# Kernel tuning notes

Hardware: AMD Instinct MI355X
Metric: run time of the kernel (lower is better)

The kernel has to match this reference:

```python
import jax, jax.numpy as jnp
import numpy as np
from jax import lax

T, B, C, H, W, NH = 4, 4, 512, 32, 32, 8
HD = C // NH  # head dim 64
EPS = 1e-5
TAU = 2.0

@jax.custom_vjp
def spike(x):
    # Heaviside forward (spikingjelly: x >= 0 -> 1)
    return (x >= 0.0).astype(x.dtype)

def _spike_fwd(x):
    return spike(x), x

def _spike_bwd(x, g):
    # sigmoid surrogate gradient, alpha=4.0 (spikingjelly default)
    s = jax.nn.sigmoid(4.0 * x)
    return (g * 4.0 * s * (1.0 - s),)

spike.defvjp(_spike_fwd, _spike_bwd)

def lif(x, v_th=1.0):
    # MultiStepLIFNode: tau=2, v_reset=0 (hard reset), detach_reset=True.
    # x: [T, ...]; sequential over T via scan.
    def step(v, xt):
        v = v + (xt - v) / TAU
        s = spike(v - v_th)
        v = v * (1.0 - lax.stop_gradient(s))  # detach_reset hard reset
        return v, s
    return lax.scan(step, jnp.zeros_like(x[0]), x)[1]

def bn(x, g, b, m, v):
    # eval-mode BatchNorm1d over channel axis 2 of [T,B,C,N]
    scale = g / jnp.sqrt(v + EPS)
    return (x - m[:, None]) * scale[:, None] + b[:, None]

def setup_inputs() -> dict:
    key = jax.random.key(0)
    ks = jax.random.split(key, 24)
    def w(k):
        return jax.random.normal(k, (C, C), jnp.float32) * (1.0 / np.sqrt(C))
    def bnp(k):
        k1, k2, k3, k4 = jax.random.split(k, 4)
        return (jax.random.normal(k1, (C,), jnp.float32) * 0.1 + 1.0,
                jax.random.normal(k2, (C,), jnp.float32) * 0.1,
                jax.random.normal(k3, (C,), jnp.float32) * 0.1,
                jax.random.uniform(k4, (C,), jnp.float32, 0.5, 1.5))
    q_g, q_b, q_m, q_v = bnp(ks[1])
    k_g, k_b, k_m, k_v = bnp(ks[3])
    v_g, v_b, v_m, v_v = bnp(ks[5])
    p_g, p_b, p_m, p_v = bnp(ks[7])
    return {
        'x': jax.random.normal(ks[0], (T, B, C, H, W), jnp.float32),
        'Wq': w(ks[10]), 'q_g': q_g, 'q_b': q_b, 'q_m': q_m, 'q_v': q_v,
        'Wk': w(ks[11]), 'k_g': k_g, 'k_b': k_b, 'k_m': k_m, 'k_v': k_v,
        'Wv': w(ks[12]), 'v_g': v_g, 'v_b': v_b, 'v_m': v_m, 'v_v': v_v,
        'Wp': w(ks[13]), 'bp': jax.random.normal(ks[14], (C,), jnp.float32) * 0.02,
        'p_g': p_g, 'p_b': p_b, 'p_m': p_m, 'p_v': p_v,
    }

def reference(x, Wq, q_g, q_b, q_m, q_v, Wk, k_g, k_b, k_m, k_v,
              Wv, v_g, v_b, v_m, v_v, Wp, bp, p_g, p_b, p_m, p_v):
    t, b, c, h, w = x.shape
    n = h * w
    xs = lif(x).reshape(t, b, c, n)  # proj_lif -> spikes in {0,1}

    def qkv_branch(Wt, g, bb, m, v):
        y = jnp.einsum('tbcn,dc->tbdn', xs, Wt)  # conv1x1
        y = lif(bn(y, g, bb, m, v))               # bn + lif
        # [T,B,C,N] -> [T,B,heads,N,head_dim]
        return y.reshape(t, b, NH, HD, n).transpose(0, 1, 2, 4, 3)

    q = qkv_branch(Wq, q_g, q_b, q_m, q_v)
    k = qkv_branch(Wk, k_g, k_b, k_m, k_v)
    v = qkv_branch(Wv, v_g, v_b, v_m, v_v)

    attn = jnp.einsum('tbhnd,tbhmd->tbhnm', q, k)           # q @ k^T (binary spikes)
    o = jnp.einsum('tbhnm,tbhmd->tbhnd', attn, v) * 0.125   # attn @ v * 0.125
    o = o.transpose(0, 1, 2, 4, 3).reshape(t, b, c, n)      # [T,B,C,N]
    o = lif(o, v_th=0.5)                                     # attn_lif

    y = jnp.einsum('tbcn,dc->tbdn', o, Wp) + bp[:, None]     # proj conv (bias)
    y = bn(y, p_g, p_b, p_m, p_v)
    return y.reshape(t, b, c, h, w)
```

## Files before the change

kernel.cpp:

```cpp
#include <hip/hip_runtime.h>
#include <hip/hip_bf16.h>
#include <stdint.h>

#define T_  4
#define B_  4
#define C_  512
#define N_  1024
#define NH_ 8
#define HD_ 64
#define NP_ 16384
#define EPS_ 1e-5f

typedef __bf16 bf16_t;
typedef __bf16 bf16x8 __attribute__((ext_vector_type(8)));
typedef float  f32x4  __attribute__((ext_vector_type(4)));
typedef unsigned short u16x4 __attribute__((ext_vector_type(4)));
typedef unsigned char  u8x4  __attribute__((ext_vector_type(4)));
typedef unsigned long long u64;
typedef unsigned int u32;

#define XS_OFF   0ULL
#define AHI_OFF  16777216ULL
#define ALO_OFF  18350080ULL
#define PHI_OFF  19922944ULL
#define PLO_OFF  20447232ULL
#define SC_OFF   20971520ULL
#define SH_OFF   20977664ULL
#define PSC_OFF  20983808ULL
#define PSH_OFF  20985856ULL
#define QS_OFF   20987904ULL
#define KB_OFF   37765120ULL
#define VB_OFF   38813696ULL
#define M2H_OFF  39862272ULL
#define M2L_OFF  40910848ULL

__global__ __launch_bounds__(256) void prep_lif_kernel(
    const float* __restrict__ x, bf16_t* __restrict__ xsT,
    const float* __restrict__ Wq, const float* __restrict__ Wk,
    const float* __restrict__ Wv, const float* __restrict__ Wp,
    const float* __restrict__ qg, const float* __restrict__ qb, const float* __restrict__ qm, const float* __restrict__ qv,
    const float* __restrict__ kg, const float* __restrict__ kb, const float* __restrict__ km, const float* __restrict__ kv,
    const float* __restrict__ vg, const float* __restrict__ vb, const float* __restrict__ vm, const float* __restrict__ vv,
    const float* __restrict__ bp,
    const float* __restrict__ pg, const float* __restrict__ pb, const float* __restrict__ pm, const float* __restrict__ pv,
    bf16_t* __restrict__ Ahi, bf16_t* __restrict__ Alo,
    bf16_t* __restrict__ Phi, bf16_t* __restrict__ Plo,
    float* __restrict__ scale, float* __restrict__ shift,
    float* __restrict__ pscale, float* __restrict__ pshift)
{
    __shared__ bf16_t St[64 * 72];
    const int tid = threadIdx.x;

    if (blockIdx.z == 4) {
        const int i0 = (blockIdx.y * 16 + blockIdx.x) * 256 + tid;
        const int stride = 128 * 256;
        for (int idx = i0; idx < 1536 * 512; idx += stride) {
            int r = idx >> 9;
            int br = r >> 9;
            const float* W = (br == 0) ? Wq : (br == 1) ? Wk : Wv;
            float w = W[((r & 511) << 9) + (idx & 511)];
            bf16_t h = (bf16_t)w;
            Ahi[idx] = h;
            Alo[idx] = (bf16_t)(w - (float)h);
        }
        for (int idx = i0; idx < 512 * 512; idx += stride) {
            float w = Wp[idx];
            bf16_t h = (bf16_t)w;
            Phi[idx] = h;
            Plo[idx] = (bf16_t)(w - (float)h);
        }
        for (int idx = i0; idx < 1536; idx += stride) {
            int br = idx >> 9, d = idx & 511;
            const float* g  = (br == 0) ? qg : (br == 1) ? kg : vg;
            const float* bb = (br == 0) ? qb : (br == 1) ? kb : vb;
            const float* mm = (br == 0) ? qm : (br == 1) ? km : vm;
            const float* vr = (br == 0) ? qv : (br == 1) ? kv : vv;
            float sc = g[d] / sqrtf(vr[d] + EPS_);
            scale[idx] = sc;
            shift[idx] = bb[d] - mm[d] * sc;
        }
        for (int idx = i0; idx < 512; idx += stride) {
            float sc = pg[idx] / sqrtf(pv[idx] + EPS_);
            pscale[idx] = sc;
            pshift[idx] = (bp[idx] - pm[idx]) * sc + pb[idx];
        }
        return;
    }

    const int nl  = tid & 63;
    const int c4  = tid >> 6;
    const int n0 = blockIdx.x * 64;
    const int c0 = blockIdx.y * 64;
    const int b  = blockIdx.z;
    float v[16];
#pragma unroll
    for (int k = 0; k < 16; ++k) v[k] = 0.f;

    for (int t = 0; t < T_; ++t) {
        bf16x8 s0, s1;
#pragma unroll
        for (int k = 0; k < 16; ++k) {
            float xv = x[(size_t)((t * B_ + b) * C_ + (c0 + c4 * 16 + k)) * N_ + n0 + nl];
            float vn = v[k] + (xv - v[k]) * 0.5f;
            bool s = (vn >= 1.0f);
            v[k] = s ? 0.0f : vn;
            bf16_t sp = s ? (bf16_t)1.0f : (bf16_t)0.0f;
            if (k < 8) s0[k] = sp; else s1[k - 8] = sp;
        }
        __syncthreads();
        *(bf16x8*)&St[nl * 72 + c4 * 16]     = s0;
        *(bf16x8*)&St[nl * 72 + c4 * 16 + 8] = s1;
        __syncthreads();
#pragma unroll
        for (int it = 0; it < 2; ++it) {
            int id = it * 256 + tid;
            int row = id >> 3, sg = id & 7;
            *(bf16x8*)&xsT[((size_t)((t * B_ + b) << 10) + n0 + row) * C_ + c0 + sg * 8] =
                *(const bf16x8*)&St[row * 72 + sg * 8];
        }
    }
}

__global__ __launch_bounds__(256) void gemm_qkv_lif(
    const bf16_t* __restrict__ Ahi, const bf16_t* __restrict__ Alo,
    const bf16_t* __restrict__ xsT,
    const float* __restrict__ scale, const float* __restrict__ shift,
    bf16_t* __restrict__ qsT, u32* __restrict__ kbits, u32* __restrict__ vbits)
{
    __shared__ __align__(16) unsigned char smem[49152];

    const int tid  = threadIdx.x;
    const int lane = tid & 63;
    const int wv   = tid >> 6;
    const int wr   = wv >> 1, wc = wv & 1;
    const int m0   = blockIdx.y * 128;
    const int branch = m0 >> 9;
    const int site0 = blockIdx.x * 32;
    const int b    = site0 >> 10;
    const int n0   = site0 & 1023;

    const int frow = lane & 15;
    const int g4   = lane >> 4;

    f32x4 acc[4][4];
#pragma unroll
    for (int t = 0; t < 4; ++t)
#pragma unroll
        for (int mi = 0; mi < 4; ++mi) acc[t][mi] = f32x4{0.f, 0.f, 0.f, 0.f};

    for (int kk = 0; kk < 512; kk += 64) {
        __syncthreads();
#pragma unroll
        for (int p = 0; p < 4; ++p) {
            int s = p * 256 + tid;
            int row = s >> 3, j = s & 7;
            int kc = (j ^ (row & 7)) << 3;
            size_t goff = (size_t)(m0 + row) * 512 + kk + kc;
            unsigned ldsb = (unsigned)(p * 256 + wv * 64) * 16;
            __builtin_amdgcn_global_load_lds((const __attribute__((address_space(1))) void*)(Ahi + goff),
                                             (__attribute__((address_space(3))) void*)(smem + ldsb), 16, 0, 0);
            __builtin_amdgcn_global_load_lds((const __attribute__((address_space(1))) void*)(Alo + goff),
                                             (__attribute__((address_space(3))) void*)(smem + 16384 + ldsb), 16, 0, 0);
        }
#pragma unroll
        for (int p = 0; p < 4; ++p) {
            int s = p * 256 + tid;
            int t = s >> 8, row = (s >> 3) & 31, j = s & 7;
            int kc = (j ^ (row & 7)) << 3;
            size_t goff = ((size_t)((t * B_ + b) << 10) + n0 + row) * 512 + kk + kc;
            unsigned ldsb = 32768u + (unsigned)(p * 256 + wv * 64) * 16;
            __builtin_amdgcn_global_load_lds((const __attribute__((address_space(1))) void*)(xsT + goff),
                                             (__attribute__((address_space(3))) void*)(smem + ldsb), 16, 0, 0);
        }
        __syncthreads();

#pragma unroll
        for (int ks = 0; ks < 2; ++ks) {
            bf16x8 ah[4], al[4];
#pragma unroll
            for (int mi = 0; mi < 4; ++mi) {
                int row = wr * 64 + mi * 16 + frow;
                int jj = (ks * 4 + g4) ^ (row & 7);
                ah[mi] = *(const bf16x8*)(smem + row * 128 + jj * 16);
                al[mi] = *(const bf16x8*)(smem + 16384 + row * 128 + jj * 16);
            }
#pragma unroll
            for (int t = 0; t < 4; ++t) {
                int rowb = wc * 16 + frow;
                int jj = (ks * 4 + g4) ^ (rowb & 7);
                bf16x8 bb = *(const bf16x8*)(smem + 32768 + t * 4096 + rowb * 128 + jj * 16);
#pragma unroll
                for (int mi = 0; mi < 4; ++mi) {
                    acc[t][mi] = __builtin_amdgcn_mfma_f32_16x16x32_bf16(ah[mi], bb, acc[t][mi], 0, 0, 0);
                    acc[t][mi] = __builtin_amdgcn_mfma_f32_16x16x32_bf16(al[mi], bb, acc[t][mi], 0, 0, 0);
                }
            }
        }
    }

    if (branch == 0) {
        bf16_t* Tt = (bf16_t*)smem;
        u16x4 qpk[4][4];
#pragma unroll
        for (int mi = 0; mi < 4; ++mi)
#pragma unroll
            for (int r = 0; r < 4; ++r) {
                int gr = m0 + wr * 64 + mi * 16 + g4 * 4 + r;
                float sc = scale[gr], sh = shift[gr];
                float vv = 0.f;
#pragma unroll
                for (int t = 0; t < 4; ++t) {
                    float y = acc[t][mi][r] * sc + sh;
                    float vn = vv + (y - vv) * 0.5f;
                    bool s = (vn >= 1.0f);
                    vv = s ? 0.f : vn;
                    qpk[t][mi][r] = s ? 0x3F80 : 0;
                }
            }
#pragma unroll
        for (int t = 0; t < 4; ++t) {
            const int tb = t * B_ + b;
            __syncthreads();
#pragma unroll
            for (int mi = 0; mi < 4; ++mi) {
                int nl = wc * 16 + frow;
                int cl = wr * 64 + mi * 16 + g4 * 4;
                *(u16x4*)&Tt[nl * 136 + cl] = qpk[t][mi];
            }
            __syncthreads();
#pragma unroll
            for (int it = 0; it < 2; ++it) {
                int id = it * 256 + tid;
                int row = id >> 4, sg = id & 15;
                *(bf16x8*)&qsT[((size_t)(tb << 10) + n0 + row) * 512 + m0 + sg * 8] =
                    *(const bf16x8*)&Tt[row * 136 + sg * 8];
            }
        }
    } else {
        unsigned char* Sb = (unsigned char*)smem;
        u32* bdst = (branch == 1) ? kbits : vbits;
        u8x4 kpk[4][4];
#pragma unroll
        for (int mi = 0; mi < 4; ++mi)
#pragma unroll
            for (int r = 0; r < 4; ++r) {
                int gr = m0 + wr * 64 + mi * 16 + g4 * 4 + r;
                float sc = scale[gr], sh = shift[gr];
                float vv = 0.f;
#pragma unroll
                for (int t = 0; t < 4; ++t) {
                    float y = acc[t][mi][r] * sc + sh;
                    float vn = vv + (y - vv) * 0.5f;
                    bool s = (vn >= 1.0f);
                    vv = s ? 0.f : vn;
                    kpk[t][mi][r] = s ? 1 : 0;
                }
            }
#pragma unroll
        for (int t = 0; t < 4; ++t) {
            const int tb = t * B_ + b;
            __syncthreads();
#pragma unroll
            for (int mi = 0; mi < 4; ++mi) {
                int nl = wc * 16 + frow;
                int cl = wr * 64 + mi * 16 + g4 * 4;
                *(u8x4*)&Sb[nl * 132 + cl] = kpk[t][mi];
            }
            __syncthreads();
#pragma unroll
            for (int i = 0; i < 16; ++i) {
                int item = wv * 16 + i;
                int c = item * 2 + (lane >> 5);
                unsigned char vb_ = Sb[(lane & 31) * 132 + c];
                u64 mask = __ballot(vb_ != 0);
                if (lane == 0) {
                    int r0 = (m0 & 511) + item * 2;
                    int r1 = r0 + 1;
                    bdst[((size_t)(tb * NH_ + (r0 >> 6)) * 64 + (r0 & 63)) * 32 + (n0 >> 5)] = (u32)mask;
                    bdst[((size_t)(tb * NH_ + (r1 >> 6)) * 64 + (r1 & 63)) * 32 + (n0 >> 5)] = (u32)(mask >> 32);
                }
            }
        }
    }
}

__global__ __launch_bounds__(256) void gemm_proj(
    const bf16_t* __restrict__ Phi, const bf16_t* __restrict__ Plo,
    const bf16_t* __restrict__ Bm,
    const float* __restrict__ scale, const float* __restrict__ shift,
    float* __restrict__ out)
{
    __shared__ __align__(16) unsigned char smem[49152];

    const int tid  = threadIdx.x;
    const int lane = tid & 63;
    const int wv   = tid >> 6;
    const int wr   = wv >> 1, wc = wv & 1;
    const int m0   = blockIdx.y * 128;
    const int n0   = blockIdx.x * 128;

    const int frow = lane & 15;
    const int g4   = lane >> 4;

    f32x4 acc[4][4];
#pragma unroll
    for (int i = 0; i < 4; ++i)
#pragma unroll
        for (int j = 0; j < 4; ++j) acc[i][j] = f32x4{0.f, 0.f, 0.f, 0.f};

    for (int kk = 0; kk < 512; kk += 64) {
        __syncthreads();
#pragma unroll
        for (int p = 0; p < 4; ++p) {
            int s = p * 256 + tid;
            int row = s >> 3, j = s & 7;
            int kc = (j ^ (row & 7)) << 3;
            size_t goff = (size_t)(m0 + row) * 512 + kk + kc;
            unsigned ldsb = (unsigned)(p * 256 + wv * 64) * 16;
            __builtin_amdgcn_global_load_lds((const __attribute__((address_space(1))) void*)(Phi + goff),
                                             (__attribute__((address_space(3))) void*)(smem + ldsb), 16, 0, 0);
            __builtin_amdgcn_global_load_lds((const __attribute__((address_space(1))) void*)(Plo + goff),
                                             (__attribute__((address_space(3))) void*)(smem + 16384 + ldsb), 16, 0, 0);
        }
#pragma unroll
        for (int p = 0; p < 4; ++p) {
            int s = p * 256 + tid;
            int row = s >> 3, j = s & 7;
            int kc = (j ^ (row & 7)) << 3;
            size_t goff = (size_t)(n0 + row) * 512 + kk + kc;
            unsigned ldsb = 32768u + (unsigned)(p * 256 + wv * 64) * 16;
            __builtin_amdgcn_global_load_lds((const __attribute__((address_space(1))) void*)(Bm + goff),
                                             (__attribute__((address_space(3))) void*)(smem + ldsb), 16, 0, 0);
        }
        __syncthreads();

#pragma unroll
        for (int ks = 0; ks < 2; ++ks) {
            bf16x8 ah[4], al[4];
#pragma unroll
            for (int mi = 0; mi < 4; ++mi) {
                int row = wr * 64 + mi * 16 + frow;
                int jj = (ks * 4 + g4) ^ (row & 7);
                ah[mi] = *(const bf16x8*)(smem + row * 128 + jj * 16);
                al[mi] = *(const bf16x8*)(smem + 16384 + row * 128 + jj * 16);
            }
#pragma unroll
            for (int ni = 0; ni < 4; ++ni) {
                int site = wc * 64 + ni * 16 + frow;
                int jj = (ks * 4 + g4) ^ (site & 7);
                bf16x8 bb = *(const bf16x8*)(smem + 32768 + site * 128 + jj * 16);
#pragma unroll
                for (int mi = 0; mi < 4; ++mi) {
                    acc[mi][ni] = __builtin_amdgcn_mfma_f32_16x16x32_bf16(ah[mi], bb, acc[mi][ni], 0, 0, 0);
                    acc[mi][ni] = __builtin_amdgcn_mfma_f32_16x16x32_bf16(al[mi], bb, acc[mi][ni], 0, 0, 0);
                }
            }
        }
    }

#pragma unroll
    for (int mi = 0; mi < 4; ++mi)
#pragma unroll
        for (int ni = 0; ni < 4; ++ni)
#pragma unroll
            for (int r = 0; r < 4; ++r) {
                int gr = m0 + wr * 64 + mi * 16 + g4 * 4 + r;
                int gc = n0 + wc * 64 + ni * 16 + frow;
                float vout = acc[mi][ni][r] * scale[gr] + shift[gr];
                int tb = gc >> 10, nn = gc & 1023;
                out[((size_t)(tb * C_ + gr)) * N_ + nn] = vout;
            }
}

__global__ __launch_bounds__(256) void m2t_kernel(const u64* __restrict__ kbit,
                                                  const u64* __restrict__ vbit,
                                                  bf16_t* __restrict__ m2h,
                                                  bf16_t* __restrict__ m2l)
{
    __shared__ u64 Kb[64][17];
    __shared__ u64 Vb[64][17];
    __shared__ float M2f[64][64];
    const int tid = threadIdx.x;
    const int h  = blockIdx.x;
    const int tb = blockIdx.y;

    const u64* kbase = kbit + (size_t)(tb * NH_ + h) * 1024;
    const u64* vbase = vbit + (size_t)(tb * NH_ + h) * 1024;
    for (int i = tid; i < 1024; i += 256) {
        Kb[i >> 4][i & 15] = kbase[i];
        Vb[i >> 4][i & 15] = vbase[i];
    }
    __syncthreads();

    const int d1 = tid >> 2, l2 = tid & 3;
    int cnt[16];
#pragma unroll
    for (int jj = 0; jj < 16; ++jj) cnt[jj] = 0;
    for (int w = 0; w < 16; ++w) {
        u64 kw = Kb[d1][w];
#pragma unroll
        for (int jj = 0; jj < 16; ++jj)
            cnt[jj] += __popcll(kw & Vb[l2 + 4 * jj][w]);
    }
#pragma unroll
    for (int jj = 0; jj < 16; ++jj)
        M2f[d1][l2 + 4 * jj] = (float)cnt[jj] * 0.125f;
    __syncthreads();

    const int d2 = tid >> 2, d1b = (tid & 3) * 16;
    bf16x8 h0, h1, l0, l1;
#pragma unroll
    for (int j = 0; j < 16; ++j) {
        float m = M2f[d1b + j][d2];
        bf16_t hi = (bf16_t)m;
        bf16_t lo = (bf16_t)(m - (float)hi);
        if (j < 8) { h0[j] = hi; l0[j] = lo; } else { h1[j - 8] = hi; l1[j - 8] = lo; }
    }
    size_t base = (size_t)(tb * NH_ + h) * 4096 + tid * 16;
    *(bf16x8*)&m2h[base]     = h0;
    *(bf16x8*)&m2h[base + 8] = h1;
    *(bf16x8*)&m2l[base]     = l0;
    *(bf16x8*)&m2l[base + 8] = l1;
}

__global__ __launch_bounds__(256) void o_kernel(const bf16_t* __restrict__ qsT,
                                                const bf16_t* __restrict__ m2h,
                                                const bf16_t* __restrict__ m2l,
                                                bf16_t* __restrict__ osT)
{
    __shared__ bf16_t Ah[64][72];
    __shared__ bf16_t Al[64][72];
    __shared__ bf16_t Bq[64][72];
    __shared__ bf16_t Ot[64][72];

    const int tid  = threadIdx.x;
    const int lane = tid & 63;
    const int wv   = tid >> 6;
    const int nt = blockIdx.x, h = blockIdx.y, b = blockIdx.z;
    const int n0 = nt * 64;
    const int frow = lane & 15;
    const int g    = lane >> 4;

    float vst[4][4];
#pragma unroll
    for (int mi = 0; mi < 4; ++mi)
#pragma unroll
        for (int r = 0; r < 4; ++r) vst[mi][r] = 0.f;

    for (int t = 0; t < T_; ++t) {
        const int tb = t * B_ + b;
        __syncthreads();
        {
            int row = tid >> 2, col = (tid & 3) * 16;
            size_t gbase = (size_t)(tb * NH_ + h) * 4096 + row * 64 + col;
            *(bf16x8*)&Ah[row][col]     = *(const bf16x8*)&m2h[gbase];
            *(bf16x8*)&Ah[row][col + 8] = *(const bf16x8*)&m2h[gbase + 8];
            *(bf16x8*)&Al[row][col]     = *(const bf16x8*)&m2l[gbase];
            *(bf16x8*)&Al[row][col + 8] = *(const bf16x8*)&m2l[gbase + 8];
        }
#pragma unroll
        for (int it = 0; it < 2; ++it) {
            int id = it * 256 + tid;
            int row = id >> 3, cg = (id & 7) * 8;
            *(bf16x8*)&Bq[row][cg] =
                *(const bf16x8*)&qsT[(size_t)((tb << 10) + n0 + row) * C_ + h * 64 + cg];
        }
        __syncthreads();

        bf16x8 afh[4][2], afl[4][2], bfq[2];
#pragma unroll
        for (int mi = 0; mi < 4; ++mi)
#pragma unroll
            for (int ks = 0; ks < 2; ++ks) {
                afh[mi][ks] = *(const bf16x8*)&Ah[mi * 16 + frow][ks * 32 + g * 8];
                afl[mi][ks] = *(const bf16x8*)&Al[mi * 16 + frow][ks * 32 + g * 8];
            }
#pragma unroll
        for (int ks = 0; ks < 2; ++ks)
            bfq[ks] = *(const bf16x8*)&Bq[wv * 16 + frow][ks * 32 + g * 8];

        f32x4 acc[4];
#pragma unroll
        for (int mi = 0; mi < 4; ++mi) acc[mi] = f32x4{0.f, 0.f, 0.f, 0.f};

#pragma unroll
        for (int ks = 0; ks < 2; ++ks)
#pragma unroll
            for (int mi = 0; mi < 4; ++mi) {
                acc[mi] = __builtin_amdgcn_mfma_f32_16x16x32_bf16(afh[mi][ks], bfq[ks], acc[mi], 0, 0, 0);
                acc[mi] = __builtin_amdgcn_mfma_f32_16x16x32_bf16(afl[mi][ks], bfq[ks], acc[mi], 0, 0, 0);
            }

#pragma unroll
        for (int mi = 0; mi < 4; ++mi) {
            u16x4 pk;
#pragma unroll
            for (int r = 0; r < 4; ++r) {
                float o = acc[mi][r];
                float vn = vst[mi][r] + (o - vst[mi][r]) * 0.5f;
                bool s = (vn >= 0.5f);
                vst[mi][r] = s ? 0.f : vn;
                pk[r] = s ? 0x3F80 : 0;
            }
            *(u16x4*)&Ot[wv * 16 + frow][mi * 16 + g * 4] = pk;
        }
        __syncthreads();

#pragma unroll
        for (int it = 0; it < 2; ++it) {
            int id = it * 256 + tid;
            int row = id >> 3, sg = (id & 7) * 8;
            *(bf16x8*)&osT[(size_t)((tb << 10) + n0 + row) * C_ + h * 64 + sg] =
                *(const bf16x8*)&Ot[row][sg];
        }
    }
}

extern "C" void kernel_launch(void* const* d_in, const int* in_sizes, int n_in,
                              void* d_out, int out_size, void* d_ws, size_t ws_size,
                              hipStream_t stream)
{
    const float* x   = (const float*)d_in[0];
    const float* Wq  = (const float*)d_in[1];
    const float* qg  = (const float*)d_in[2];
    const float* qb  = (const float*)d_in[3];
    const float* qm  = (const float*)d_in[4];
    const float* qv  = (const float*)d_in[5];
    const float* Wk  = (const float*)d_in[6];
    const float* kg  = (const float*)d_in[7];
    const float* kb  = (const float*)d_in[8];
    const float* km  = (const float*)d_in[9];
    const float* kv  = (const float*)d_in[10];
    const float* Wv  = (const float*)d_in[11];
    const float* vg  = (const float*)d_in[12];
    const float* vb  = (const float*)d_in[13];
    const float* vm  = (const float*)d_in[14];
    const float* vv  = (const float*)d_in[15];
    const float* Wp  = (const float*)d_in[16];
    const float* bp  = (const float*)d_in[17];
    const float* pg  = (const float*)d_in[18];
    const float* pb  = (const float*)d_in[19];
    const float* pm  = (const float*)d_in[20];
    const float* pv  = (const float*)d_in[21];

    char* ws = (char*)d_ws;
    bf16_t* xsT    = (bf16_t*)(ws + XS_OFF);
    bf16_t* Ahi    = (bf16_t*)(ws + AHI_OFF);
    bf16_t* Alo    = (bf16_t*)(ws + ALO_OFF);
    bf16_t* Phi    = (bf16_t*)(ws + PHI_OFF);
    bf16_t* Plo    = (bf16_t*)(ws + PLO_OFF);
    float*  scv    = (float*)(ws + SC_OFF);
    float*  shv    = (float*)(ws + SH_OFF);
    float*  psc    = (float*)(ws + PSC_OFF);
    float*  psh    = (float*)(ws + PSH_OFF);
    bf16_t* qsT    = (bf16_t*)(ws + QS_OFF);
    u32*    kbits32= (u32*)(ws + KB_OFF);
    u32*    vbits32= (u32*)(ws + VB_OFF);
    u64*    kbits  = (u64*)(ws + KB_OFF);
    u64*    vbits  = (u64*)(ws + VB_OFF);
    bf16_t* m2h    = (bf16_t*)(ws + M2H_OFF);
    bf16_t* m2l    = (bf16_t*)(ws + M2L_OFF);
    bf16_t* osT    = (bf16_t*)(ws + XS_OFF);
    float*  out    = (float*)d_out;

    prep_lif_kernel<<<dim3(16, 8, 5), dim3(256), 0, stream>>>(
        x, xsT, Wq, Wk, Wv, Wp, qg, qb, qm, qv, kg, kb, km, kv, vg, vb, vm, vv,
        bp, pg, pb, pm, pv, Ahi, Alo, Phi, Plo, scv, shv, psc, psh);

    gemm_qkv_lif<<<dim3(128, 12), dim3(256), 0, stream>>>(
        Ahi, Alo, xsT, scv, shv, qsT, kbits32, vbits32);

    m2t_kernel<<<dim3(8, 16), dim3(256), 0, stream>>>(kbits, vbits, m2h, m2l);

    o_kernel<<<dim3(16, 8, 4), dim3(256), 0, stream>>>(qsT, m2h, m2l, osT);

    gemm_proj<<<dim3(128, 4), dim3(256), 0, stream>>>(Phi, Plo, osT, psc, psh, out);

    (void)in_sizes; (void)n_in; (void)out_size; (void)ws_size;
}
```

Measured before the change: 213.8 us.

## Double-buffer LDS tiles in QKV and projection GEMMs to overlap loads with MFMA

```diff
diff --git a/kernel.cpp b/kernel.cpp
--- a/kernel.cpp
+++ b/kernel.cpp
@@ -127,7 +127,7 @@
     const float* __restrict__ scale, const float* __restrict__ shift,
     bf16_t* __restrict__ qsT, u32* __restrict__ kbits, u32* __restrict__ vbits)
 {
-    __shared__ __align__(16) unsigned char smem[49152];
+    __shared__ __align__(16) unsigned char smem[98304];
 
     const int tid  = threadIdx.x;
     const int lane = tid & 63;
@@ -148,8 +148,8 @@
 #pragma unroll
         for (int mi = 0; mi < 4; ++mi) acc[t][mi] = f32x4{0.f, 0.f, 0.f, 0.f};
 
-    for (int kk = 0; kk < 512; kk += 64) {
-        __syncthreads();
+    auto stage = [&](int buf, int kk) {
+        unsigned char* base = smem + buf * 49152;
 #pragma unroll
         for (int p = 0; p < 4; ++p) {
             int s = p * 256 + tid;
@@ -158,9 +158,9 @@
             size_t goff = (size_t)(m0 + row) * 512 + kk + kc;
             unsigned ldsb = (unsigned)(p * 256 + wv * 64) * 16;
             __builtin_amdgcn_global_load_lds((const __attribute__((address_space(1))) void*)(Ahi + goff),
-                                             (__attribute__((address_space(3))) void*)(smem + ldsb), 16, 0, 0);
+                                             (__attribute__((address_space(3))) void*)(base + ldsb), 16, 0, 0);
             __builtin_amdgcn_global_load_lds((const __attribute__((address_space(1))) void*)(Alo + goff),
-                                             (__attribute__((address_space(3))) void*)(smem + 16384 + ldsb), 16, 0, 0);
+                                             (__attribute__((address_space(3))) void*)(base + 16384 + ldsb), 16, 0, 0);
         }
 #pragma unroll
         for (int p = 0; p < 4; ++p) {
@@ -170,10 +170,17 @@
             size_t goff = ((size_t)((t * B_ + b) << 10) + n0 + row) * 512 + kk + kc;
             unsigned ldsb = 32768u + (unsigned)(p * 256 + wv * 64) * 16;
             __builtin_amdgcn_global_load_lds((const __attribute__((address_space(1))) void*)(xsT + goff),
-                                             (__attribute__((address_space(3))) void*)(smem + ldsb), 16, 0, 0);
-        }
-        __syncthreads();
-
+                                             (__attribute__((address_space(3))) void*)(base + ldsb), 16, 0, 0);
+        }
+    };
+
+    stage(0, 0);
+    __syncthreads();
+    int cur = 0;
+    for (int step = 0; step < 8; ++step) {
+        if (step < 7) stage(cur ^ 1, (step + 1) * 64);
+
+        unsigned char* base = smem + cur * 49152;
 #pragma unroll
         for (int ks = 0; ks < 2; ++ks) {
             bf16x8 ah[4], al[4];
@@ -181,14 +188,14 @@
             for (int mi = 0; mi < 4; ++mi) {
                 int row = wr * 64 + mi * 16 + frow;
                 int jj = (ks * 4 + g4) ^ (row & 7);
-                ah[mi] = *(const bf16x8*)(smem + row * 128 + jj * 16);
-                al[mi] = *(const bf16x8*)(smem + 16384 + row * 128 + jj * 16);
+                ah[mi] = *(const bf16x8*)(base + row * 128 + jj * 16);
+                al[mi] = *(const bf16x8*)(base + 16384 + row * 128 + jj * 16);
             }
 #pragma unroll
             for (int t = 0; t < 4; ++t) {
                 int rowb = wc * 16 + frow;
                 int jj = (ks * 4 + g4) ^ (rowb & 7);
-                bf16x8 bb = *(const bf16x8*)(smem + 32768 + t * 4096 + rowb * 128 + jj * 16);
+                bf16x8 bb = *(const bf16x8*)(base + 32768 + t * 4096 + rowb * 128 + jj * 16);
 #pragma unroll
                 for (int mi = 0; mi < 4; ++mi) {
                     acc[t][mi] = __builtin_amdgcn_mfma_f32_16x16x32_bf16(ah[mi], bb, acc[t][mi], 0, 0, 0);
@@ -196,6 +203,8 @@
                 }
             }
         }
+        __syncthreads();
+        cur ^= 1;
     }
 
     if (branch == 0) {
@@ -290,7 +299,7 @@
     const float* __restrict__ scale, const float* __restrict__ shift,
     float* __restrict__ out)
 {
-    __shared__ __align__(16) unsigned char smem[49152];
+    __shared__ __align__(16) unsigned char smem[98304];
 
     const int tid  = threadIdx.x;
     const int lane = tid & 63;
@@ -308,8 +317,8 @@
 #pragma unroll
         for (int j = 0; j < 4; ++j) acc[i][j] = f32x4{0.f, 0.f, 0.f, 0.f};
 
-    for (int kk = 0; kk < 512; kk += 64) {
-        __syncthreads();
+    auto stage = [&](int buf, int kk) {
+        unsigned char* base = smem + buf * 49152;
 #pragma unroll
         for (int p = 0; p < 4; ++p) {
             int s = p * 256 + tid;
@@ -318,9 +327,9 @@
             size_t goff = (size_t)(m0 + row) * 512 + kk + kc;
             unsigned ldsb = (unsigned)(p * 256 + wv * 64) * 16;
             __builtin_amdgcn_global_load_lds((const __attribute__((address_space(1))) void*)(Phi + goff),
-                                             (__attribute__((address_space(3))) void*)(smem + ldsb), 16, 0, 0);
+                                             (__attribute__((address_space(3))) void*)(base + ldsb), 16, 0, 0);
             __builtin_amdgcn_global_load_lds((const __attribute__((address_space(1))) void*)(Plo + goff),
-                                             (__attribute__((address_space(3))) void*)(smem + 16384 + ldsb), 16, 0, 0);
+                                             (__attribute__((address_space(3))) void*)(base + 16384 + ldsb), 16, 0, 0);
         }
 #pragma unroll
         for (int p = 0; p < 4; ++p) {
@@ -330,10 +339,17 @@
             size_t goff = (size_t)(n0 + row) * 512 + kk + kc;
             unsigned ldsb = 32768u + (unsigned)(p * 256 + wv * 64) * 16;
             __builtin_amdgcn_global_load_lds((const __attribute__((address_space(1))) void*)(Bm + goff),
-                                             (__attribute__((address_space(3))) void*)(smem + ldsb), 16, 0, 0);
-        }
-        __syncthreads();
-
+                                             (__attribute__((address_space(3))) void*)(base + ldsb), 16, 0, 0);
+        }
+    };
+
+    stage(0, 0);
+    __syncthreads();
+    int cur = 0;
+    for (int step = 0; step < 8; ++step) {
+        if (step < 7) stage(cur ^ 1, (step + 1) * 64);
+
+        unsigned char* base = smem + cur * 49152;
 #pragma unroll
         for (int ks = 0; ks < 2; ++ks) {
             bf16x8 ah[4], al[4];
@@ -341,14 +357,14 @@
             for (int mi = 0; mi < 4; ++mi) {
                 int row = wr * 64 + mi * 16 + frow;
                 int jj = (ks * 4 + g4) ^ (row & 7);
-                ah[mi] = *(const bf16x8*)(smem + row * 128 + jj * 16);
-                al[mi] = *(const bf16x8*)(smem + 16384 + row * 128 + jj * 16);
+                ah[mi] = *(const bf16x8*)(base + row * 128 + jj * 16);
+                al[mi] = *(const bf16x8*)(base + 16384 + row * 128 + jj * 16);
             }
 #pragma unroll
             for (int ni = 0; ni < 4; ++ni) {
                 int site = wc * 64 + ni * 16 + frow;
                 int jj = (ks * 4 + g4) ^ (site & 7);
-                bf16x8 bb = *(const bf16x8*)(smem + 32768 + site * 128 + jj * 16);
+                bf16x8 bb = *(const bf16x8*)(base + 32768 + site * 128 + jj * 16);
 #pragma unroll
                 for (int mi = 0; mi < 4; ++mi) {
                     acc[mi][ni] = __builtin_amdgcn_mfma_f32_16x16x32_bf16(ah[mi], bb, acc[mi][ni], 0, 0, 0);
@@ -356,6 +372,8 @@
                 }
             }
         }
+        __syncthreads();
+        cur ^= 1;
     }
 
 #pragma unroll
```

Result: slower. 239.8 us (+12.2%).
